# Performance work log

Hardware: AMD Instinct MI355X
Metric: run time of the kernel (lower is better)

The kernel has to match this reference:

```python
import jax, jax.numpy as jnp
import numpy as np

EMB = 256

def setup_inputs() -> dict:
    key = jax.random.key(0)
    ks = jax.random.split(key, 7)
    c = EMB
    x = jax.random.normal(ks[0], (4, c, 64, 64), dtype=jnp.float32)
    s = 1.0 / np.sqrt(c)
    Wq = jax.random.uniform(ks[1], (c, c), jnp.float32, -s, s)
    bq = jax.random.uniform(ks[2], (c,), jnp.float32, -s, s)
    Wk = jax.random.uniform(ks[3], (c, c), jnp.float32, -s, s)
    bk = jax.random.uniform(ks[4], (c,), jnp.float32, -s, s)
    Wv = jax.random.uniform(ks[5], (c, c), jnp.float32, -s, s)
    bv = jax.random.uniform(ks[6], (c,), jnp.float32, -s, s)
    return {"x": x, "Wq": Wq, "bq": bq, "Wk": Wk, "bk": bk, "Wv": Wv, "bv": bv}

def reference(x, Wq, bq, Wk, bk, Wv, bv):
    b, c, h, w = x.shape
    scale = jnp.sqrt(jnp.float32(c))
    # [b, n, c] tokens, n = h*w
    xt = x.reshape(b, c, h * w).transpose(0, 2, 1)
    q = jnp.einsum('bnc,dc->bnd', xt, Wq) + bq
    k = jnp.einsum('bnc,dc->bnd', xt, Wk) + bk
    v = jnp.einsum('bnc,dc->bnd', xt, Wv) + bv
    dist = jnp.einsum('bnd,bmd->bnm', q, k) / scale  # [b, n, n]
    dist = jax.nn.softmax(dist, axis=-1)
    mem = jnp.einsum('bnm,bmd->bnd', dist, v)  # [b, n, c]
    # Original: permute(0,1,2) is identity, then raw view(b,c,h,w) -> reshape
    return mem.reshape(b, c, h, w)
```

## Files before the change

### kernel.cpp

```cpp
#include <hip/hip_runtime.h>

typedef __attribute__((ext_vector_type(8))) short short8;
typedef __attribute__((ext_vector_type(4))) short short4_t;
typedef __attribute__((ext_vector_type(4))) float float4_t;
typedef __attribute__((ext_vector_type(16))) float float16_t;
typedef __attribute__((ext_vector_type(2))) int int2_t;

#define NTOK 4096
#define CDIM 256
#define BPB (NTOK * CDIM)
#define C1 0.0901684400555602f

__device__ inline float bf2f(short s) {
    return __uint_as_float(((unsigned)(unsigned short)s) << 16);
}
__device__ inline short f2bf(float f) {
    unsigned u = __float_as_uint(f);
    return (short)((u + 0x7fffu + ((u >> 16) & 1u)) >> 16);
}
__device__ inline int cvtpk_bf16(float lo, float hi) {
    int d;
    asm("v_cvt_pk_bf16_f32 %0, %1, %2" : "=v"(d) : "v"(lo), "v"(hi));
    return d;
}
__device__ inline void gl_lds16(const void* g, void* l) {
    __builtin_amdgcn_global_load_lds(
        (const __attribute__((address_space(1))) unsigned int*)g,
        (__attribute__((address_space(3))) unsigned int*)l, 16, 0, 0);
}

__global__ void sniff_dtype(const unsigned* __restrict__ x, int* __restrict__ flag) {
    __shared__ int cnt;
    if (threadIdx.x == 0) cnt = 0;
    __syncthreads();
    int local = 0;
    for (int i = threadIdx.x; i < 1024; i += 256) {
        unsigned e = (x[i] >> 7) & 0xffu;
        if (e >= 100u && e <= 140u) local++;
    }
    atomicAdd(&cnt, local);
    __syncthreads();
    if (threadIdx.x == 0) flag[0] = (cnt >= 512) ? 1 : 0;
}

__global__ __launch_bounds__(256) void wprep(
    const void* __restrict__ Wq, const void* __restrict__ Wk,
    const void* __restrict__ Wv, const int* __restrict__ flag,
    short* __restrict__ Wb)
{
    const int base = (blockIdx.x * 256 + threadIdx.x) * 8;
    const int wsel = base >> 16, off = base & 65535;
    const void* W = (wsel == 0) ? Wq : (wsel == 1) ? Wk : Wv;
    short8 v;
    if (flag[0]) {
        v = *(const short8*)((const short*)W + off);
    } else {
        const float* f = (const float*)W + off;
        float4 a = *(const float4*)f;
        float4 c4 = *(const float4*)(f + 4);
        v[0]=f2bf(a.x);  v[1]=f2bf(a.y);  v[2]=f2bf(a.z);  v[3]=f2bf(a.w);
        v[4]=f2bf(c4.x); v[5]=f2bf(c4.y); v[6]=f2bf(c4.z); v[7]=f2bf(c4.w);
    }
    *(short8*)(Wb + base) = v;
}

template <bool PIN>
__global__ __launch_bounds__(256, 3) void qkv6(
    const void* __restrict__ xv, const short* __restrict__ Wb,
    const void* __restrict__ bq, const void* __restrict__ bk,
    const void* __restrict__ bv,
    const int* __restrict__ flag, int b0,
    short* __restrict__ qbase, short* __restrict__ kbase,
    short* __restrict__ vtbase)
{
    int nt, bl, wsel;
    if (PIN) {
        const int bid = blockIdx.x;
        wsel = bid >> 8;
        const int rem = bid & 255;
        bl = rem & 3; nt = rem >> 2;
    } else { nt = blockIdx.x; wsel = blockIdx.y; bl = blockIdx.z; }
    const int b = b0 + bl;
    const int n0 = nt * 64;
    const int tid = threadIdx.x;
    const int w = tid >> 6, lane = tid & 63, l15 = lane & 15, qd = lane >> 4;
    const int isbf = flag[0];

    __shared__ short xt[64 * 264];

    {
        const size_t xb = (size_t)b * CDIM * NTOK + (size_t)tid * NTOK + n0;
        if (isbf) {
            const short* x = (const short*)xv;
            #pragma unroll
            for (int i = 0; i < 8; ++i) {
                short8 v = *(const short8*)(x + xb + i * 8);
                #pragma unroll
                for (int j = 0; j < 8; ++j) xt[(i * 8 + j) * 264 + tid] = v[j];
            }
        } else {
            const float* x = (const float*)xv;
            #pragma unroll
            for (int i = 0; i < 16; ++i) {
                float4 v = *(const float4*)(x + xb + i * 4);
                xt[(i * 4 + 0) * 264 + tid] = f2bf(v.x);
                xt[(i * 4 + 1) * 264 + tid] = f2bf(v.y);
                xt[(i * 4 + 2) * 264 + tid] = f2bf(v.z);
                xt[(i * 4 + 3) * 264 + tid] = f2bf(v.w);
            }
        }
    }
    __syncthreads();

    short8 af[8];
    #pragma unroll
    for (int s = 0; s < 8; ++s)
        af[s] = *(const short8*)&xt[(16 * w + l15) * 264 + s * 32 + qd * 8];

    const short* W = Wb + wsel * 65536;
    const void* bp = (wsel == 0) ? bq : (wsel == 1) ? bk : bv;
    short* qdst  = qbase  + (size_t)bl * BPB;
    short* kdst  = kbase  + (size_t)bl * BPB;
    short* vtdst = vtbase + (size_t)bl * BPB;

    #pragma unroll 2
    for (int dg = 0; dg < 16; ++dg) {
        const int d = dg * 16 + l15;
        const short* wr = W + (size_t)d * 256 + qd * 8;
        short8 wv[8];
        #pragma unroll
        for (int s = 0; s < 8; ++s) wv[s] = *(const short8*)(wr + s * 32);
        float4_t acc = {0.f, 0.f, 0.f, 0.f};
        #pragma unroll
        for (int s = 0; s < 8; ++s)
            acc = __builtin_amdgcn_mfma_f32_16x16x32_bf16(af[s], wv[s], acc, 0, 0, 0);
        const float bias = isbf ? bf2f(((const short*)bp)[d])
                                : ((const float*)bp)[d];
        if (wsel == 0) {
            #pragma unroll
            for (int r = 0; r < 4; ++r) {
                const int n = n0 + 16 * w + 4 * qd + r;
                qdst[(size_t)n * 256 + d] = f2bf(acc[r] + bias);
            }
        } else if (wsel == 1) {
            #pragma unroll
            for (int r = 0; r < 4; ++r) {
                const int n = n0 + 16 * w + 4 * qd + r;
                const int rl = n & 31;
                kdst[((size_t)(n >> 5)) * 8192 + rl * 256
                     + (((d >> 3) ^ rl) * 8) + (d & 7)] = f2bf(acc[r] + bias);
            }
        } else {
            short4_t pk;
            #pragma unroll
            for (int r = 0; r < 4; ++r) pk[r] = f2bf(acc[r] + bias);
            const int n = n0 + 16 * w + 4 * qd;
            const int kl = n & 31;
            *(short4_t*)(vtdst + ((size_t)(n >> 5)) * 8192 + d * 32
                         + (((kl >> 3) ^ (d & 3)) * 8) + (kl & 7)) = pk;
        }
    }
}

template <bool PIN, bool SPLIT>
__global__ __launch_bounds__(256, 2) void flash11(
    int b0, const short* __restrict__ qb, const short* __restrict__ kb,
    const short* __restrict__ vtb, const int* __restrict__ flag,
    void* __restrict__ outv, float* __restrict__ pO, float* __restrict__ pl)
{
    int qt, bl, half;
    if (SPLIT) {
        const int bid = blockIdx.x;
        bl = (bid >> 1) & 3; half = bid & 1; qt = bid >> 3;
    } else if (PIN) {
        bl = blockIdx.x & 3; qt = blockIdx.x >> 2; half = 0;
    } else { qt = blockIdx.x; bl = blockIdx.z; half = 0; }

    const int b = b0 + bl;
    const int q0 = qt * 64;
    const int tid = threadIdx.x;
    const int w = tid >> 6, lane = tid & 63, l31 = lane & 31, h = lane >> 5;
    const int wi = w & 1, wh = w >> 1;

    __shared__ __align__(16) char smem[67584];
    short* kbufA = (short*)smem;
    short* vbufA = (short*)(smem + 32768);

    const short* Q  = qb  + (size_t)bl * BPB;
    const char*  Kc = (const char*)(kb  + (size_t)bl * BPB);
    const char*  Vc = (const char*)(vtb + (size_t)bl * BPB);

    short8 qf[16];
    {
        const short* qrow = Q + (size_t)(q0 + 32 * wh + l31) * 256 + h * 8;
        #pragma unroll
        for (int s = 0; s < 16; ++s)
            qf[s] = *(const short8*)(qrow + s * 16);
    }

    float16_t oacc[4];
    #pragma unroll
    for (int dt = 0; dt < 4; ++dt)
        #pragma unroll
        for (int r = 0; r < 16; ++r) oacc[dt][r] = 0.f;
    float lloc = 0.f;

    const int KT0 = SPLIT ? half * 64 : 0;
    const int KT1 = KT0 + (SPLIT ? 64 : 128);

    {
        const char* ks = Kc + ((size_t)KT0 << 14);
        const char* vs = Vc + ((size_t)KT0 << 14);
        char* kd = smem + tid * 16;
        char* vd = smem + 32768 + tid * 16;
        #pragma unroll
        for (int u = 0; u < 4; ++u) {
            gl_lds16(ks + u * 4096 + tid * 16, kd + u * 4096);
            gl_lds16(vs + u * 4096 + tid * 16, vd + u * 4096);
        }
    }
    __syncthreads();

    #pragma unroll 1
    for (int kt = KT0; kt < KT1; ++kt) {
        short* kcur = kbufA + (kt & 1) * 8192;
        short* vcur = vbufA + (kt & 1) * 8192;

        if (kt + 1 < KT1) {
            const int alt = (kt + 1) & 1;
            const char* ks = Kc + ((size_t)(kt + 1) << 14);
            const char* vs = Vc + ((size_t)(kt + 1) << 14);
            char* kd = smem + alt * 16384 + tid * 16;
            char* vd = smem + 32768 + alt * 16384 + tid * 16;
            #pragma unroll
            for (int u = 0; u < 4; ++u) {
                gl_lds16(ks + u * 4096 + tid * 16, kd + u * 4096);
                gl_lds16(vs + u * 4096 + tid * 16, vd + u * 4096);
            }
        }

        float16_t se, so;
        #pragma unroll
        for (int r = 0; r < 16; ++r) { se[r] = 0.f; so[r] = 0.f; }
        #pragma unroll
        for (int j = 0; j < 8; ++j) {
            short8 ka = *(const short8*)
                &kcur[l31 * 256 + (((4 * j + h) ^ l31) * 8)];
            se = __builtin_amdgcn_mfma_f32_32x32x16_bf16(ka, qf[2 * j], se, 0, 0, 0);
            short8 kb2 = *(const short8*)
                &kcur[l31 * 256 + (((4 * j + 2 + h) ^ l31) * 8)];
            so = __builtin_amdgcn_mfma_f32_32x32x16_bf16(kb2, qf[2 * j + 1], so, 0, 0, 0);
        }

        float pf[16];
        #pragma unroll
        for (int r = 0; r < 16; ++r) {
            pf[r] = exp2f((se[r] + so[r]) * C1);
            lloc += pf[r];
        }

        short8 pa[2];
        #pragma unroll
        for (int s2 = 0; s2 < 2; ++s2) {
            const int bse = s2 * 8;
            int x  = cvtpk_bf16(pf[bse + 0], pf[bse + 1]);
            int y  = cvtpk_bf16(pf[bse + 4], pf[bse + 5]);
            int z  = cvtpk_bf16(pf[bse + 2], pf[bse + 3]);
            int u2 = cvtpk_bf16(pf[bse + 6], pf[bse + 7]);
            int2_t r1 = __builtin_amdgcn_permlane32_swap(x, y, false, false);
            int2_t r2 = __builtin_amdgcn_permlane32_swap(z, u2, false, false);
            union { int i[4]; short8 s8; } uu;
            uu.i[0] = r1[0]; uu.i[1] = r2[0]; uu.i[2] = r1[1]; uu.i[3] = r2[1];
            pa[s2] = uu.s8;
        }

        #pragma unroll
        for (int dt = 0; dt < 4; ++dt) {
            const int d = 128 * wi + 32 * dt + l31;
            #pragma unroll
            for (int s2 = 0; s2 < 2; ++s2) {
                short8 vf = *(const short8*)
                    &vcur[d * 32 + (((2 * s2 + h) ^ (d & 3)) * 8)];
                oacc[dt] = __builtin_amdgcn_mfma_f32_32x32x16_bf16(pa[s2], vf, oacc[dt], 0, 0, 0);
            }
        }

        __syncthreads();
    }

    float* lbuf = (float*)(smem + 66560);
    {
        float v2 = lloc + __shfl_xor(lloc, 32, 64);
        if (h == 0 && wi == 0) lbuf[32 * wh + l31] = v2;
    }

    if (SPLIT) {
        const size_t pidx = (size_t)(bl * 64 + qt) * 2 + half;
        float* po = pO + pidx * 16384;
        #pragma unroll
        for (int dt = 0; dt < 4; ++dt) {
            const int dim = 128 * wi + 32 * dt + l31;
            #pragma unroll
            for (int r = 0; r < 16; ++r) {
                const int qrow = 32 * wh + (r & 3) + 8 * (r >> 2) + 4 * h;
                po[qrow * 256 + dim] = oacc[dt][r];
            }
        }
        __syncthreads();
        if (tid < 64) pl[pidx * 64 + tid] = lbuf[tid];
    } else {
        float* obuf = (float*)smem;
        #pragma unroll
        for (int dt = 0; dt < 4; ++dt) {
            const int dim = 128 * wi + 32 * dt + l31;
            #pragma unroll
            for (int r = 0; r < 16; ++r) {
                const int qrow = 32 * wh + (r & 3) + 8 * (r >> 2) + 4 * h;
                obuf[qrow * 260 + dim] = oacc[dt][r];
            }
        }
        __syncthreads();
        {
            const int row = tid >> 2, q4 = (tid & 3) * 64;
            const float inv = 1.0f / lbuf[row];
            const float* src = obuf + row * 260 + q4;
            const size_t o = (size_t)(b * NTOK + q0 + row) * 256 + q4;
            if (flag[0]) {
                short* op = (short*)outv;
                #pragma unroll
                for (int g = 0; g < 4; ++g) {
                    float4 a  = *(const float4*)(src + g * 8);
                    float4 c4 = *(const float4*)(src + g * 8 + 4);
                    short8 pk;
                    pk[0]=f2bf(a.x*inv);  pk[1]=f2bf(a.y*inv);
                    pk[2]=f2bf(a.z*inv);  pk[3]=f2bf(a.w*inv);
                    pk[4]=f2bf(c4.x*inv); pk[5]=f2bf(c4.y*inv);
                    pk[6]=f2bf(c4.z*inv); pk[7]=f2bf(c4.w*inv);
                    *(short8*)(op + o + g * 8) = pk;
                }
            } else {
                float* op = (float*)outv;
                #pragma unroll
                for (int g = 0; g < 16; ++g) {
                    float4 a = *(const float4*)(src + g * 4);
                    a.x *= inv; a.y *= inv; a.z *= inv; a.w *= inv;
                    *(float4*)(op + o + g * 4) = a;
                }
            }
        }
    }
}

__global__ __launch_bounds__(256) void combine(
    const float* __restrict__ pO, const float* __restrict__ pl,
    const int* __restrict__ flag, void* __restrict__ outv)
{
    const int tile = blockIdx.x, tid = threadIdx.x;
    const int row = tid >> 2, seg = (tid & 3) * 64;
    const float* A = pO + (size_t)tile * 32768 + row * 256 + seg;
    const float* B = A + 16384;
    const float inv = 1.0f / (pl[tile * 128 + row] + pl[tile * 128 + 64 + row]);
    const size_t o = ((size_t)tile * 64 + row) * 256 + seg;
    if (flag[0]) {
        short* op = (short*)outv;
        #pragma unroll
        for (int g = 0; g < 8; ++g) {
            float4 a  = *(const float4*)(A + g * 8);
            float4 a2 = *(const float4*)(A + g * 8 + 4);
            float4 c  = *(const float4*)(B + g * 8);
            float4 c2 = *(const float4*)(B + g * 8 + 4);
            short8 pk;
            pk[0]=f2bf((a.x+c.x)*inv);   pk[1]=f2bf((a.y+c.y)*inv);
            pk[2]=f2bf((a.z+c.z)*inv);   pk[3]=f2bf((a.w+c.w)*inv);
            pk[4]=f2bf((a2.x+c2.x)*inv); pk[5]=f2bf((a2.y+c2.y)*inv);
            pk[6]=f2bf((a2.z+c2.z)*inv); pk[7]=f2bf((a2.w+c2.w)*inv);
            *(short8*)(op + o + g * 8) = pk;
        }
    } else {
        float* op = (float*)outv;
        #pragma unroll
        for (int g = 0; g < 16; ++g) {
            float4 a = *(const float4*)(A + g * 4);
            float4 c = *(const float4*)(B + g * 4);
            a.x = (a.x + c.x) * inv; a.y = (a.y + c.y) * inv;
            a.z = (a.z + c.z) * inv; a.w = (a.w + c.w) * inv;
            *(float4*)(op + o + g * 4) = a;
        }
    }
}

extern "C" void kernel_launch(void* const* d_in, const int* in_sizes, int n_in,
                              void* d_out, int out_size, void* d_ws, size_t ws_size,
                              hipStream_t stream)
{
    const size_t HDR = 256;
    const size_t WBB = 393216;
    const size_t TB  = (size_t)BPB * 2;
    const size_t OFF_K = HDR + WBB;
    const size_t need_prim  = OFF_K + 12 * TB;
    const size_t need_split = need_prim + 33554432 + 131072;

    int*   flag = (int*)d_ws;
    short* Wb   = (short*)((char*)d_ws + HDR);

    sniff_dtype<<<1, 256, 0, stream>>>((const unsigned*)d_in[0], flag);
    wprep<<<96, 256, 0, stream>>>(d_in[1], d_in[3], d_in[5], flag, Wb);

    if (ws_size >= need_prim) {
        short* kbase  = (short*)((char*)d_ws + OFF_K);
        short* vtbase = kbase  + 4 * (size_t)BPB;
        short* qbase  = vtbase + 4 * (size_t)BPB;
        qkv6<true><<<dim3(768, 1, 1), 256, 0, stream>>>(
            d_in[0], Wb, d_in[2], d_in[4], d_in[6], flag, 0,
            qbase, kbase, vtbase);
        if (ws_size >= need_split) {
            float* pO = (float*)((char*)d_ws + need_prim);
            float* pl = (float*)((char*)d_ws + need_prim + 33554432);
            flash11<true, true><<<dim3(512, 1, 1), 256, 0, stream>>>(
                0, qbase, kbase, vtbase, flag, d_out, pO, pl);
            combine<<<dim3(256, 1, 1), 256, 0, stream>>>(pO, pl, flag, d_out);
        } else {
            flash11<true, false><<<dim3(256, 1, 1), 256, 0, stream>>>(
                0, qbase, kbase, vtbase, flag, d_out, nullptr, nullptr);
        }
        return;
    }

    int nb = 4;
    while (nb > 1 && ws_size < OFF_K + (size_t)nb * 3 * TB) nb--;
    short* kbase  = (short*)((char*)d_ws + OFF_K);
    short* vtbase = kbase + (size_t)nb * BPB;
    short* qbase  = vtbase + (size_t)nb * BPB;

    for (int b0 = 0; b0 < 4; b0 += nb) {
        const int nbc = (4 - b0) < nb ? (4 - b0) : nb;
        qkv6<false><<<dim3(64, 3, nbc), 256, 0, stream>>>(
            d_in[0], Wb, d_in[2], d_in[4], d_in[6], flag, b0,
            qbase, kbase, vtbase);
        flash11<false, false><<<dim3(64, 1, nbc), 256, 0, stream>>>(
            b0, qbase, kbase, vtbase, flag, d_out, nullptr, nullptr);
    }
}
```

Measured before the change: 267.8 us.

## Software-pipeline PV matmul one tile behind QK and stage QKV stores via LDS

The flash kernel now issues the P·V MFMAs for the previous key tile while the current tile's QK scores are computed, and splits the K and V prefetches so V is loaded after a mid-iteration barrier. The V^T layout and its swizzle are reworked to match. The QKV projection kernel loads x straight into registers with strided gathers instead of transposing through LDS. It stages outputs in LDS so the Q, K and V^T writes become coalesced 16-byte stores. The strided x gathers may cost more global traffic, and the extra barrier and carried P registers raise pressure in the flash loop.

Result: no change. 269.8 us (+0.8%).

```diff
diff --git a/kernel.cpp b/kernel.cpp
--- a/kernel.cpp
+++ b/kernel.cpp
@@ -65,7 +65,7 @@
 }
 
 template <bool PIN>
-__global__ __launch_bounds__(256, 3) void qkv6(
+__global__ __launch_bounds__(256, 3) void qkv7(
     const void* __restrict__ xv, const short* __restrict__ Wb,
     const void* __restrict__ bq, const void* __restrict__ bk,
     const void* __restrict__ bv,
@@ -86,42 +86,36 @@
     const int w = tid >> 6, lane = tid & 63, l15 = lane & 15, qd = lane >> 4;
     const int isbf = flag[0];
 
-    __shared__ short xt[64 * 264];
-
+    __shared__ short obuf[64 * 264];
+
+    short8 af[8];
     {
-        const size_t xb = (size_t)b * CDIM * NTOK + (size_t)tid * NTOK + n0;
+        const int n = n0 + 16 * w + l15;
         if (isbf) {
-            const short* x = (const short*)xv;
-            #pragma unroll
-            for (int i = 0; i < 8; ++i) {
-                short8 v = *(const short8*)(x + xb + i * 8);
+            const short* xs = (const short*)xv + (size_t)b * CDIM * NTOK + n;
+            #pragma unroll
+            for (int s = 0; s < 8; ++s) {
+                short8 v;
                 #pragma unroll
-                for (int j = 0; j < 8; ++j) xt[(i * 8 + j) * 264 + tid] = v[j];
+                for (int e = 0; e < 8; ++e)
+                    v[e] = xs[(size_t)(s * 32 + qd * 8 + e) * NTOK];
+                af[s] = v;
             }
         } else {
-            const float* x = (const float*)xv;
-            #pragma unroll
-            for (int i = 0; i < 16; ++i) {
-                float4 v = *(const float4*)(x + xb + i * 4);
-                xt[(i * 4 + 0) * 264 + tid] = f2bf(v.x);
-                xt[(i * 4 + 1) * 264 + tid] = f2bf(v.y);
-                xt[(i * 4 + 2) * 264 + tid] = f2bf(v.z);
-                xt[(i * 4 + 3) * 264 + tid] = f2bf(v.w);
-            }
-        }
-    }
-    __syncthreads();
-
-    short8 af[8];
-    #pragma unroll
-    for (int s = 0; s < 8; ++s)
-        af[s] = *(const short8*)&xt[(16 * w + l15) * 264 + s * 32 + qd * 8];
+            const float* xf = (const float*)xv + (size_t)b * CDIM * NTOK + n;
+            #pragma unroll
+            for (int s = 0; s < 8; ++s) {
+                short8 v;
+                #pragma unroll
+                for (int e = 0; e < 8; ++e)
+                    v[e] = f2bf(xf[(size_t)(s * 32 + qd * 8 + e) * NTOK]);
+                af[s] = v;
+            }
+        }
+    }
 
     const short* W = Wb + wsel * 65536;
     const void* bp = (wsel == 0) ? bq : (wsel == 1) ? bk : bv;
-    short* qdst  = qbase  + (size_t)bl * BPB;
-    short* kdst  = kbase  + (size_t)bl * BPB;
-    short* vtdst = vtbase + (size_t)bl * BPB;
 
     #pragma unroll 2
     for (int dg = 0; dg < 16; ++dg) {
@@ -136,34 +130,53 @@
             acc = __builtin_amdgcn_mfma_f32_16x16x32_bf16(af[s], wv[s], acc, 0, 0, 0);
         const float bias = isbf ? bf2f(((const short*)bp)[d])
                                 : ((const float*)bp)[d];
-        if (wsel == 0) {
-            #pragma unroll
-            for (int r = 0; r < 4; ++r) {
-                const int n = n0 + 16 * w + 4 * qd + r;
-                qdst[(size_t)n * 256 + d] = f2bf(acc[r] + bias);
-            }
-        } else if (wsel == 1) {
-            #pragma unroll
-            for (int r = 0; r < 4; ++r) {
-                const int n = n0 + 16 * w + 4 * qd + r;
-                const int rl = n & 31;
-                kdst[((size_t)(n >> 5)) * 8192 + rl * 256
-                     + (((d >> 3) ^ rl) * 8) + (d & 7)] = f2bf(acc[r] + bias);
-            }
+        if (wsel < 2) {
+            #pragma unroll
+            for (int r = 0; r < 4; ++r)
+                obuf[(16 * w + 4 * qd + r) * 264 + d] = f2bf(acc[r] + bias);
         } else {
-            short4_t pk;
-            #pragma unroll
-            for (int r = 0; r < 4; ++r) pk[r] = f2bf(acc[r] + bias);
-            const int n = n0 + 16 * w + 4 * qd;
-            const int kl = n & 31;
-            *(short4_t*)(vtdst + ((size_t)(n >> 5)) * 8192 + d * 32
-                         + (((kl >> 3) ^ (d & 3)) * 8) + (kl & 7)) = pk;
+            #pragma unroll
+            for (int r = 0; r < 4; ++r)
+                obuf[d * 66 + (16 * w + 4 * qd + r)] = f2bf(acc[r] + bias);
+        }
+    }
+    __syncthreads();
+
+    if (wsel == 0) {
+        short* qdst = qbase + (size_t)bl * BPB;
+        const int rl = tid >> 2;
+        #pragma unroll
+        for (int u = 0; u < 8; ++u) {
+            const int cc = (tid & 3) + 4 * u;
+            short8 vv = *(const short8*)&obuf[rl * 264 + cc * 8];
+            *(short8*)(qdst + (size_t)(n0 + rl) * 256 + cc * 8) = vv;
+        }
+    } else if (wsel == 1) {
+        short* kdst = kbase + (size_t)bl * BPB;
+        const int rl = tid >> 2;
+        const int tile = (n0 + rl) >> 5, rit = rl & 31;
+        #pragma unroll
+        for (int u = 0; u < 8; ++u) {
+            const int ccp = (tid & 3) + 4 * u;
+            const int cc  = ccp ^ rit;
+            short8 vv = *(const short8*)&obuf[rl * 264 + cc * 8];
+            *(short8*)(kdst + (size_t)tile * 8192 + rit * 256 + ccp * 8) = vv;
+        }
+    } else {
+        short* vtdst = vtbase + (size_t)bl * BPB;
+        const int d = tid;
+        #pragma unroll
+        for (int u = 0; u < 8; ++u) {
+            short8 vv = *(const short8*)&obuf[d * 66 + u * 8];
+            const int tile = (n0 >> 5) + (u >> 2), ck = u & 3;
+            const int pos = ((d & 1) * 4 + ck) ^ ((d >> 1) & 7);
+            *(short8*)(vtdst + (size_t)tile * 8192 + (d >> 1) * 64 + pos * 8) = vv;
         }
     }
 }
 
 template <bool PIN, bool SPLIT>
-__global__ __launch_bounds__(256, 2) void flash11(
+__global__ __launch_bounds__(256, 2) void flash12(
     int b0, const short* __restrict__ qb, const short* __restrict__ kb,
     const short* __restrict__ vtb, const int* __restrict__ flag,
     void* __restrict__ outv, float* __restrict__ pO, float* __restrict__ pl)
@@ -185,6 +198,7 @@
     __shared__ __align__(16) char smem[67584];
     short* kbufA = (short*)smem;
     short* vbufA = (short*)(smem + 32768);
+    float* lbuf  = (float*)(smem + 66560);
 
     const short* Q  = qb  + (size_t)bl * BPB;
     const char*  Kc = (const char*)(kb  + (size_t)bl * BPB);
@@ -203,7 +217,7 @@
     for (int dt = 0; dt < 4; ++dt)
         #pragma unroll
         for (int r = 0; r < 16; ++r) oacc[dt][r] = 0.f;
-    float lloc = 0.f;
+    float ll0 = 0.f, ll1 = 0.f, ll2 = 0.f, ll3 = 0.f;
 
     const int KT0 = SPLIT ? half * 64 : 0;
     const int KT1 = KT0 + (SPLIT ? 64 : 128);
@@ -221,22 +235,19 @@
     }
     __syncthreads();
 
+    short8 pa0 = {0,0,0,0,0,0,0,0}, pa1 = {0,0,0,0,0,0,0,0};
+
     #pragma unroll 1
     for (int kt = KT0; kt < KT1; ++kt) {
-        short* kcur = kbufA + (kt & 1) * 8192;
-        short* vcur = vbufA + (kt & 1) * 8192;
+        short* kcur  = kbufA + (kt & 1) * 8192;
+        short* vprev = vbufA + ((kt + 1) & 1) * 8192;
 
         if (kt + 1 < KT1) {
-            const int alt = (kt + 1) & 1;
             const char* ks = Kc + ((size_t)(kt + 1) << 14);
-            const char* vs = Vc + ((size_t)(kt + 1) << 14);
-            char* kd = smem + alt * 16384 + tid * 16;
-            char* vd = smem + 32768 + alt * 16384 + tid * 16;
-            #pragma unroll
-            for (int u = 0; u < 4; ++u) {
+            char* kd = smem + (((kt + 1) & 1) << 14) + tid * 16;
+            #pragma unroll
+            for (int u = 0; u < 4; ++u)
                 gl_lds16(ks + u * 4096 + tid * 16, kd + u * 4096);
-                gl_lds16(vs + u * 4096 + tid * 16, vd + u * 4096);
-            }
         }
 
         float16_t se, so;
@@ -252,45 +263,89 @@
             so = __builtin_amdgcn_mfma_f32_32x32x16_bf16(kb2, qf[2 * j + 1], so, 0, 0, 0);
         }
 
+        if (kt > KT0) {
+            #pragma unroll
+            for (int dt = 0; dt < 4; ++dt) {
+                const int d = 128 * wi + 32 * dt + l31, d2 = d >> 1;
+                {
+                    const int pos = (((d & 1) * 4 + h) ^ (d2 & 7));
+                    short8 vf = *(const short8*)&vprev[d2 * 64 + pos * 8];
+                    oacc[dt] = __builtin_amdgcn_mfma_f32_32x32x16_bf16(pa0, vf, oacc[dt], 0, 0, 0);
+                }
+                {
+                    const int pos = (((d & 1) * 4 + 2 + h) ^ (d2 & 7));
+                    short8 vf = *(const short8*)&vprev[d2 * 64 + pos * 8];
+                    oacc[dt] = __builtin_amdgcn_mfma_f32_32x32x16_bf16(pa1, vf, oacc[dt], 0, 0, 0);
+                }
+            }
+        }
+
+        asm volatile("s_waitcnt lgkmcnt(0)" ::: "memory");
+        __builtin_amdgcn_sched_barrier(0);
+        __builtin_amdgcn_s_barrier();
+        __builtin_amdgcn_sched_barrier(0);
+
+        if (kt + 1 < KT1) {
+            const char* vs = Vc + ((size_t)(kt + 1) << 14);
+            char* vd = smem + 32768 + (((kt + 1) & 1) << 14) + tid * 16;
+            #pragma unroll
+            for (int u = 0; u < 4; ++u)
+                gl_lds16(vs + u * 4096 + tid * 16, vd + u * 4096);
+        }
+
         float pf[16];
         #pragma unroll
-        for (int r = 0; r < 16; ++r) {
-            pf[r] = exp2f((se[r] + so[r]) * C1);
-            lloc += pf[r];
-        }
-
-        short8 pa[2];
-        #pragma unroll
-        for (int s2 = 0; s2 < 2; ++s2) {
-            const int bse = s2 * 8;
-            int x  = cvtpk_bf16(pf[bse + 0], pf[bse + 1]);
-            int y  = cvtpk_bf16(pf[bse + 4], pf[bse + 5]);
-            int z  = cvtpk_bf16(pf[bse + 2], pf[bse + 3]);
-            int u2 = cvtpk_bf16(pf[bse + 6], pf[bse + 7]);
-            int2_t r1 = __builtin_amdgcn_permlane32_swap(x, y, false, false);
-            int2_t r2 = __builtin_amdgcn_permlane32_swap(z, u2, false, false);
+        for (int r = 0; r < 16; ++r) pf[r] = exp2f((se[r] + so[r]) * C1);
+        #pragma unroll
+        for (int g = 0; g < 4; ++g) {
+            ll0 += pf[4 * g + 0]; ll1 += pf[4 * g + 1];
+            ll2 += pf[4 * g + 2]; ll3 += pf[4 * g + 3];
+        }
+        {
+            int x0 = cvtpk_bf16(pf[0], pf[1]);
+            int y0 = cvtpk_bf16(pf[4], pf[5]);
+            int z0 = cvtpk_bf16(pf[2], pf[3]);
+            int u0 = cvtpk_bf16(pf[6], pf[7]);
+            int2_t r1 = __builtin_amdgcn_permlane32_swap(x0, y0, false, false);
+            int2_t r2 = __builtin_amdgcn_permlane32_swap(z0, u0, false, false);
             union { int i[4]; short8 s8; } uu;
             uu.i[0] = r1[0]; uu.i[1] = r2[0]; uu.i[2] = r1[1]; uu.i[3] = r2[1];
-            pa[s2] = uu.s8;
-        }
-
+            pa0 = uu.s8;
+            int x1 = cvtpk_bf16(pf[8],  pf[9]);
+            int y1 = cvtpk_bf16(pf[12], pf[13]);
+            int z1 = cvtpk_bf16(pf[10], pf[11]);
+            int u1 = cvtpk_bf16(pf[14], pf[15]);
+            int2_t r3 = __builtin_amdgcn_permlane32_swap(x1, y1, false, false);
+            int2_t r4 = __builtin_amdgcn_permlane32_swap(z1, u1, false, false);
+            union { int i[4]; short8 s8; } vv;
+            vv.i[0] = r3[0]; vv.i[1] = r4[0]; vv.i[2] = r3[1]; vv.i[3] = r4[1];
+            pa1 = vv.s8;
+        }
+
+        __syncthreads();
+    }
+
+    {
+        short* vlast = vbufA + 8192;
         #pragma unroll
         for (int dt = 0; dt < 4; ++dt) {
-            const int d = 128 * wi + 32 * dt + l31;
-            #pragma unroll
-            for (int s2 = 0; s2 < 2; ++s2) {
-                short8 vf = *(const short8*)
-                    &vcur[d * 32 + (((2 * s2 + h) ^ (d & 3)) * 8)];
-                oacc[dt] = __builtin_amdgcn_mfma_f32_32x32x16_bf16(pa[s2], vf, oacc[dt], 0, 0, 0);
-            }
-        }
-
-        __syncthreads();
-    }
-
-    float* lbuf = (float*)(smem + 66560);
+            const int d = 128 * wi + 32 * dt + l31, d2 = d >> 1;
+            {
+                const int pos = (((d & 1) * 4 + h) ^ (d2 & 7));
+                short8 vf = *(const short8*)&vlast[d2 * 64 + pos * 8];
+                oacc[dt] = __builtin_amdgcn_mfma_f32_32x32x16_bf16(pa0, vf, oacc[dt], 0, 0, 0);
+            }
+            {
+                const int pos = (((d & 1) * 4 + 2 + h) ^ (d2 & 7));
+                short8 vf = *(const short8*)&vlast[d2 * 64 + pos * 8];
+                oacc[dt] = __builtin_amdgcn_mfma_f32_32x32x16_bf16(pa1, vf, oacc[dt], 0, 0, 0);
+            }
+        }
+    }
+
     {
-        float v2 = lloc + __shfl_xor(lloc, 32, 64);
+        float v2 = (ll0 + ll1) + (ll2 + ll3);
+        v2 += __shfl_xor(v2, 32, 64);
         if (h == 0 && wi == 0) lbuf[32 * wh + l31] = v2;
     }
 
@@ -309,6 +364,7 @@
         __syncthreads();
         if (tid < 64) pl[pidx * 64 + tid] = lbuf[tid];
     } else {
+        __syncthreads();
         float* obuf = (float*)smem;
         #pragma unroll
         for (int dt = 0; dt < 4; ++dt) {
@@ -410,17 +466,17 @@
         short* kbase  = (short*)((char*)d_ws + OFF_K);
         short* vtbase = kbase  + 4 * (size_t)BPB;
         short* qbase  = vtbase + 4 * (size_t)BPB;
-        qkv6<true><<<dim3(768, 1, 1), 256, 0, stream>>>(
+        qkv7<true><<<dim3(768, 1, 1), 256, 0, stream>>>(
             d_in[0], Wb, d_in[2], d_in[4], d_in[6], flag, 0,
             qbase, kbase, vtbase);
         if (ws_size >= need_split) {
             float* pO = (float*)((char*)d_ws + need_prim);
             float* pl = (float*)((char*)d_ws + need_prim + 33554432);
-            flash11<true, true><<<dim3(512, 1, 1), 256, 0, stream>>>(
+            flash12<true, true><<<dim3(512, 1, 1), 256, 0, stream>>>(
                 0, qbase, kbase, vtbase, flag, d_out, pO, pl);
             combine<<<dim3(256, 1, 1), 256, 0, stream>>>(pO, pl, flag, d_out);
         } else {
-            flash11<true, false><<<dim3(256, 1, 1), 256, 0, stream>>>(
+            flash12<true, false><<<dim3(256, 1, 1), 256, 0, stream>>>(
                 0, qbase, kbase, vtbase, flag, d_out, nullptr, nullptr);
         }
         return;
@@ -434,10 +490,10 @@
 
     for (int b0 = 0; b0 < 4; b0 += nb) {
         const int nbc = (4 - b0) < nb ? (4 - b0) : nb;
-        qkv6<false><<<dim3(64, 3, nbc), 256, 0, stream>>>(
+        qkv7<false><<<dim3(64, 3, nbc), 256, 0, stream>>>(
             d_in[0], Wb, d_in[2], d_in[4], d_in[6], flag, b0,
             qbase, kbase, vtbase);
-        flash11<false, false><<<dim3(64, 1, nbc), 256, 0, stream>>>(
+        flash12<false, false><<<dim3(64, 1, nbc), 256, 0, stream>>>(
             b0, qbase, kbase, vtbase, flag, d_out, nullptr, nullptr);
     }
 }
```
